# Kernel optimization log

Measured on AMD Instinct MI355X. Metric: run time of the kernel, lower is better.

Reference implementation:

```python
import jax, jax.numpy as jnp
import numpy as np

GW_EPS = 0.05
GW_SIGMA = 1.0
GW_OUTER_ITERS = 5
GW_SINK_ITERS = 20
N_HEADS = 8
EPS = 1e-8


def normalize_affinity(P):
    # symmetrize, scale to [0,1]
    P = 0.5 * (P + jnp.swapaxes(P, -1, -2))
    mx = jnp.max(P, axis=(-2, -1), keepdims=True)
    return P / jnp.maximum(mx, EPS)


def entropic_gw(C1, C2, a, b, eps, outer_iters, sink_iters):
    # C1: [B,H,S,S] node-space cost, C2: [B,H,K,K] slot-space cost
    # a: [B,H,S], b: [B,H,K] marginals. Square-loss entropic GW (Peyre et al.)
    T = a[..., :, None] * b[..., None, :]                      # [B,H,S,K]
    cC1 = jnp.einsum('bhij,bhj->bhi', C1 * C1, a)              # [B,H,S]
    cC2 = jnp.einsum('bhk,bhkl->bhl', b, C2 * C2)              # [B,H,K]
    const = cC1[..., :, None] + cC2[..., None, :]              # [B,H,S,K]
    tens = const
    for _ in range(outer_iters):
        tens = const - 2.0 * jnp.einsum('bhis,bhsk,bhlk->bhil', C1, T, C2)
        Kmat = jnp.exp(-tens / eps)
        u = jnp.ones_like(a)
        v = jnp.ones_like(b)
        def sink_step(carry, _):
            u, v = carry
            u = a / jnp.maximum(jnp.einsum('bhik,bhk->bhi', Kmat, v), 1e-30)
            v = b / jnp.maximum(jnp.einsum('bhik,bhi->bhk', Kmat, u), 1e-30)
            return (u, v), None
        (u, v), _ = jax.lax.scan(sink_step, (u, v), None, length=sink_iters)
        T = u[..., :, None] * Kmat * v[..., None, :]
    gw_val = jnp.sum(tens * T, axis=(-2, -1))                  # [B,H]
    return T, gw_val


def _forward(desc_embeddings, name_value_embeddings, shared_attn, prior_Q, DG, b, v_w, v_b):
    B, new_seq, D = name_value_embeddings.shape
    S = new_seq - 1
    H = N_HEADS
    hd = D // H

    # structural adjacency: CLS->Var on, Var->CLS off, Var-Var without self-loop
    var_adj = 1.0 - jnp.eye(S, dtype=name_value_embeddings.dtype)
    adj = jnp.zeros((new_seq, new_seq), dtype=name_value_embeddings.dtype)
    adj = adj.at[1:, 1:].set(var_adj)
    adj = adj.at[0, 1:].set(1.0)

    # Var-Var affinity from shared attention (detached in original)
    P_var = jax.lax.stop_gradient(shared_attn[:, :, 1:, 1:])   # [B,H,S,S]
    P_norm = normalize_affinity(P_var)
    DP = 1.0 - P_norm                                          # affinity -> distance

    deg_P = 0.5 * (P_norm.sum(-1) + P_norm.sum(-2))            # [B,H,S]
    a = deg_P / jnp.maximum(deg_P.sum(-1, keepdims=True), EPS)

    _, gw_val = entropic_gw(DP, DG, a, b, GW_EPS, GW_OUTER_ITERS, GW_SINK_ITERS)
    alpha = jnp.exp(-gw_val / GW_SIGMA)                        # [B,H] in (0,1]

    # sharpen prior Q by alpha (power sharpening + row renorm)
    Q_hat = jnp.power(jnp.maximum(prior_Q, EPS), 1.0 + alpha[..., None, None])
    Q_hat = Q_hat / jnp.maximum(Q_hat.sum(-1, keepdims=True), EPS)

    # embed Q_hat into CLS-augmented attention, mask, row-normalize
    slot = jnp.zeros((B, H, new_seq, new_seq), dtype=Q_hat.dtype)
    slot = slot.at[:, :, 1:, 1:].set(Q_hat)
    slot = slot.at[:, :, 0, 1:].set(1.0)
    slot = slot * adj[None, None]
    attn = slot / jnp.maximum(slot.sum(-1, keepdims=True), EPS)  # [B,H,S1,S1]

    v = name_value_embeddings @ v_w.T + v_b                    # [B,S1,D]
    v = v.reshape(B, new_seq, H, hd).transpose(0, 2, 1, 3)     # [B,H,S1,hd]
    context = jnp.einsum('bhij,bhjd->bhid', attn, v)
    basis_outputs = context.transpose(0, 2, 1, 3)              # [B,S1,H,hd]
    return basis_outputs, attn


def setup_inputs() -> dict:
    key = jax.random.key(0)
    ks = jax.random.split(key, 8)
    B, S1, D, H, K = 32, 385, 256, 8, 16
    S = S1 - 1
    desc = jax.random.normal(ks[0], (B, S, D), jnp.float32)
    nv = jax.random.normal(ks[1], (B, S1, D), jnp.float32)
    shared_attn = jax.nn.softmax(jax.random.normal(ks[2], (B, H, S1, S1), jnp.float32), axis=-1)
    prior_Q = jax.nn.softmax(jax.random.normal(ks[3], (B, H, S, S), jnp.float32), axis=-1)
    DG = jax.random.uniform(ks[4], (B, H, K, K), jnp.float32)
    DG = 0.5 * (DG + jnp.swapaxes(DG, -1, -2))
    b = jax.random.uniform(ks[5], (B, H, K), jnp.float32) + 0.1
    b = b / b.sum(-1, keepdims=True)
    v_w = jax.random.normal(ks[6], (D, D), jnp.float32) * (1.0 / np.sqrt(D))
    v_b = jnp.zeros((D,), jnp.float32)
    return {"desc_embeddings": desc, "name_value_embeddings": nv, "shared_attn": shared_attn,
            "prior_Q": prior_Q, "DG": DG, "b": b, "v_w": v_w, "v_b": v_b}


def reference(desc_embeddings, name_value_embeddings, shared_attn, prior_Q, DG, b, v_w, v_b):
    return _forward(desc_embeddings, name_value_embeddings, shared_attn, prior_Q, DG, b, v_w, v_b)
```

## Files before the change

### kernel.cpp

```cpp
#include <hip/hip_runtime.h>
#include <math.h>

constexpr int kS  = 384;
constexpr int kS1 = 385;
constexpr int kH  = 8;
constexpr int kB  = 32;
constexpr int kD  = 256;
constexpr float kEPS = 1e-8f;
constexpr float kNEG_INV_EPS_LOG2E = 28.853900817779268f;

__device__ __forceinline__ float waveReduceSum(float v) {
    #pragma unroll
    for (int m = 1; m < 64; m <<= 1) v += __shfl_xor(v, m);
    return v;
}
__device__ __forceinline__ float waveReduceMax(float v) {
    #pragma unroll
    for (int m = 1; m < 64; m <<= 1) v = fmaxf(v, __shfl_xor(v, m));
    return v;
}

__device__ __forceinline__ size_t symBase(int head) {
    return (size_t)head * (kS1 * kS1) + (size_t)((4 - (head & 3)) & 3);
}

__global__ __launch_bounds__(256) void k1a_sym(
    const float* __restrict__ shared_attn,
    float* __restrict__ sym_ws)
{
    const int head = blockIdx.y;
    const int ti   = blockIdx.x;
    const int tid  = threadIdx.x;
    const int c    = tid & 63;
    const int w    = tid >> 6;

    __shared__ float tB[64 * 65];
    __shared__ float wredA[4];

    const float* P = shared_attn + (size_t)head * (kS1 * kS1);
    float* SYM = sym_ws + symBase(head);
    float* rs  = SYM + kS * kS;
    float* mxs = rs + kS;

    float rs_part[16];
    #pragma unroll
    for (int k = 0; k < 16; ++k) rs_part[k] = 0.f;
    float mymax = 0.f;

    for (int tj = 0; tj < 6; ++tj) {
        __syncthreads();
        for (int e = tid; e < 4096; e += 256) {
            int r = e >> 6, cc = e & 63;
            tB[r * 65 + cc] = P[(size_t)(1 + tj * 64 + r) * kS1 + (1 + ti * 64 + cc)];
        }
        __syncthreads();
        #pragma unroll
        for (int k = 0; k < 16; ++k) {
            int r = w + 4 * k;
            float av = P[(size_t)(1 + ti * 64 + r) * kS1 + (1 + tj * 64 + c)];
            float v  = 0.5f * (av + tB[c * 65 + r]);
            mymax = fmaxf(mymax, v);
            rs_part[k] += v;
            SYM[(size_t)(ti * 64 + r) * kS + tj * 64 + c] = v;
        }
    }
    #pragma unroll
    for (int k = 0; k < 16; ++k) {
        float s = waveReduceSum(rs_part[k]);
        if (c == 0) rs[ti * 64 + w + 4 * k] = s;
    }
    float wm = waveReduceMax(mymax);
    if (c == 0) wredA[w] = wm;
    __syncthreads();
    if (tid == 0)
        mxs[ti] = fmaxf(fmaxf(wredA[0], wredA[1]), fmaxf(wredA[2], wredA[3]));
}

__global__ __launch_bounds__(384) void k1b_gw(
    const float* __restrict__ DG,
    const float* __restrict__ bmarg,
    float* __restrict__ sym_ws,
    float* __restrict__ alpha_out)
{
    const int head = blockIdx.x;
    const int tid  = threadIdx.x;
    const int lane = tid & 63, wid = tid >> 6;

    __shared__ __align__(16) float Ms[kS * 16];
    __shared__ float ravu[kS];
    __shared__ float part[6 * 16];
    __shared__ float C2l[256];
    __shared__ float bl16[16], cb16[16], cC216[16], vls[16];
    __shared__ float wred[6];

    float* SYM = sym_ws + symBase(head);
    const float* rs  = SYM + kS * kS;
    const float* mxp = rs + kS;

    if (tid < 256) C2l[tid] = DG[head * 256 + tid];
    if (tid >= 256 && tid < 272) bl16[tid - 256] = bmarg[head * 16 + (tid - 256)];

    const float tloc = rs[tid];
    float tw = waveReduceSum(tloc);
    if (lane == 0) wred[wid] = tw;
    __syncthreads();
    const float total = wred[0] + wred[1] + wred[2] + wred[3] + wred[4] + wred[5];
    const float mx = fmaxf(fmaxf(fmaxf(mxp[0], mxp[1]), fmaxf(mxp[2], mxp[3])),
                           fmaxf(mxp[4], mxp[5]));
    const float den_mx = fmaxf(mx, kEPS);
    const float inv_mx = 1.0f / den_mx;
    const float Sdeg   = total * inv_mx;
    const float den_a  = fmaxf(Sdeg, kEPS);
    const float a_reg  = (tloc * inv_mx) / den_a;
    ravu[tid] = a_reg;

    if (tid < 16) {
        float cb = 0.f, cc2 = 0.f;
        #pragma unroll
        for (int k = 0; k < 16; ++k) {
            cb += bl16[k] * C2l[tid * 16 + k];
            float c2 = C2l[k * 16 + tid];
            cc2 = fmaf(bl16[k] * c2, c2, cc2);
        }
        cb16[tid] = cb; cC216[tid] = cc2;
    }
    __syncthreads();

    const float4* __restrict__ symrow = (const float4*)(SYM + (size_t)tid * kS);
    float t1 = 0.f, t2 = 0.f;
    #pragma unroll 4
    for (int s4 = 0; s4 < 96; ++s4) {
        float4 v4 = symrow[s4];
        const float* av = &ravu[s4 * 4];
        float dp;
        dp = fmaf(-inv_mx, v4.x, 1.0f); t1 = fmaf(dp, av[0], t1); t2 = fmaf(dp * dp, av[0], t2);
        dp = fmaf(-inv_mx, v4.y, 1.0f); t1 = fmaf(dp, av[1], t1); t2 = fmaf(dp * dp, av[1], t2);
        dp = fmaf(-inv_mx, v4.z, 1.0f); t1 = fmaf(dp, av[2], t1); t2 = fmaf(dp * dp, av[2], t2);
        dp = fmaf(-inv_mx, v4.w, 1.0f); t1 = fmaf(dp, av[3], t1); t2 = fmaf(dp * dp, av[3], t2);
    }
    const float cc1 = t2;

    float kreg[16], vreg[16];
    float u_i = 0.f;
    #pragma unroll
    for (int l = 0; l < 16; ++l)
        kreg[l] = exp2f((cc1 + cC216[l] - 2.0f * cb16[l] * t1) * (-kNEG_INV_EPS_LOG2E));

    auto sinkhorn = [&]() {
        #pragma unroll
        for (int l = 0; l < 16; ++l) vreg[l] = 1.0f;
        for (int it = 0; it < 20; ++it) {
            float su = 0.f;
            #pragma unroll
            for (int l = 0; l < 16; ++l) su = fmaf(kreg[l], vreg[l], su);
            u_i = a_reg / fmaxf(su, 1e-30f);
            #pragma unroll
            for (int l = 0; l < 16; ++l) {
                float t = waveReduceSum(kreg[l] * u_i);
                if (lane == 0) part[wid * 16 + l] = t;
            }
            __syncthreads();
            if (tid < 16) {
                float dn = part[tid] + part[16 + tid] + part[32 + tid] +
                           part[48 + tid] + part[64 + tid] + part[80 + tid];
                vls[tid] = bl16[tid] / fmaxf(dn, 1e-30f);
            }
            __syncthreads();
            #pragma unroll
            for (int l = 0; l < 16; ++l) vreg[l] = vls[l];
        }
    };

    sinkhorn();

    float tens16[16];
    #pragma unroll
    for (int l = 0; l < 16; ++l) tens16[l] = 0.f;

    for (int outer = 1; outer < 5; ++outer) {
        {
            float wk[16];
            #pragma unroll
            for (int k = 0; k < 16; ++k) wk[k] = kreg[k] * vreg[k];
            float m[16];
            #pragma unroll
            for (int l = 0; l < 16; ++l) {
                float acc = 0.f;
                #pragma unroll
                for (int k = 0; k < 16; ++k) acc = fmaf(wk[k], C2l[l * 16 + k], acc);
                m[l] = acc * u_i;
            }
            float4* Ms4w = (float4*)Ms;
            Ms4w[tid * 4 + 0] = make_float4(m[0],  m[1],  m[2],  m[3]);
            Ms4w[tid * 4 + 1] = make_float4(m[4],  m[5],  m[6],  m[7]);
            Ms4w[tid * 4 + 2] = make_float4(m[8],  m[9],  m[10], m[11]);
            Ms4w[tid * 4 + 3] = make_float4(m[12], m[13], m[14], m[15]);
        }
        __syncthreads();
        float rd[16];
        #pragma unroll
        for (int l = 0; l < 16; ++l) rd[l] = 0.f;
        {
            const float4* Ms4 = (const float4*)Ms;
            #pragma unroll 2
            for (int s4 = 0; s4 < 96; ++s4) {
                float4 v4 = symrow[s4];
                #pragma unroll
                for (int j = 0; j < 4; ++j) {
                    float sym = (j == 0) ? v4.x : (j == 1) ? v4.y : (j == 2) ? v4.z : v4.w;
                    float dp = fmaf(-inv_mx, sym, 1.0f);
                    const int s = s4 * 4 + j;
                    float4 m0 = Ms4[s * 4 + 0];
                    float4 m1 = Ms4[s * 4 + 1];
                    float4 m2 = Ms4[s * 4 + 2];
                    float4 m3 = Ms4[s * 4 + 3];
                    rd[0]  = fmaf(dp, m0.x, rd[0]);  rd[1]  = fmaf(dp, m0.y, rd[1]);
                    rd[2]  = fmaf(dp, m0.z, rd[2]);  rd[3]  = fmaf(dp, m0.w, rd[3]);
                    rd[4]  = fmaf(dp, m1.x, rd[4]);  rd[5]  = fmaf(dp, m1.y, rd[5]);
                    rd[6]  = fmaf(dp, m1.z, rd[6]);  rd[7]  = fmaf(dp, m1.w, rd[7]);
                    rd[8]  = fmaf(dp, m2.x, rd[8]);  rd[9]  = fmaf(dp, m2.y, rd[9]);
                    rd[10] = fmaf(dp, m2.z, rd[10]); rd[11] = fmaf(dp, m2.w, rd[11]);
                    rd[12] = fmaf(dp, m3.x, rd[12]); rd[13] = fmaf(dp, m3.y, rd[13]);
                    rd[14] = fmaf(dp, m3.z, rd[14]); rd[15] = fmaf(dp, m3.w, rd[15]);
                }
            }
        }
        #pragma unroll
        for (int l = 0; l < 16; ++l) {
            float tens = cc1 + cC216[l] - 2.0f * rd[l];
            if (outer == 4) tens16[l] = tens;
            kreg[l] = exp2f(tens * (-kNEG_INV_EPS_LOG2E));
        }
        sinkhorn();
    }

    float g = 0.f;
    #pragma unroll
    for (int l = 0; l < 16; ++l) g = fmaf(tens16[l] * kreg[l], vreg[l], g);
    g *= u_i;
    float gww = waveReduceSum(g);
    if (lane == 0) wred[wid] = gww;
    __syncthreads();
    if (tid == 0) {
        float gw = wred[0] + wred[1] + wred[2] + wred[3] + wred[4] + wred[5];
        alpha_out[head] = expf(-gw);
    }
}

__global__ __launch_bounds__(256) void k2_attn(
    const float* __restrict__ priorQ,
    const float* __restrict__ alpha_in,
    float* __restrict__ attn_out)
{
    const int tid  = threadIdx.x;
    const int lane = tid & 63, wid = tid >> 6;
    const int head = blockIdx.x / 97;
    const int i    = (blockIdx.x % 97) * 4 + wid;
    if (i >= kS1) return;
    float* row = attn_out + (size_t)head * (kS1 * kS1) + (size_t)i * kS1;
    if (i == 0) {
        const float val = 1.0f / 384.0f;
        for (int j = lane; j < kS1; j += 64) row[j] = (j == 0) ? 0.f : val;
        return;
    }
    const float e = 1.0f + alpha_in[head];
    const float* q = priorQ + (size_t)head * (kS * kS) + (size_t)(i - 1) * kS;
    float p[6];
    float loc = 0.f, locd = 0.f;
    #pragma unroll
    for (int k = 0; k < 6; ++k) {
        int j = lane + k * 64;
        float qv = fmaxf(q[j], kEPS);
        float pv = exp2f(e * log2f(qv));
        p[k] = pv;
        loc += pv;
        if (j == i - 1) locd = pv;
    }
    float sum = loc, pd = locd;
    #pragma unroll
    for (int m = 1; m < 64; m <<= 1) { sum += __shfl_xor(sum, m); pd += __shfl_xor(pd, m); }
    const float qsum  = fmaxf(sum, kEPS);
    const float srow  = (sum - pd) / qsum;
    const float scale = 1.0f / (qsum * fmaxf(srow, kEPS));
    if (lane == 0) row[0] = 0.f;
    #pragma unroll
    for (int k = 0; k < 6; ++k) {
        int j = lane + k * 64;
        row[1 + j] = (j == i - 1) ? 0.f : p[k] * scale;
    }
}

__global__ __launch_bounds__(256) void k3_vproj(
    const float* __restrict__ nv,
    const float* __restrict__ vw,
    const float* __restrict__ vb,
    float* __restrict__ vfull)
{
    __shared__ float At[64][17];
    __shared__ float Bt[256][17];
    const int tid = threadIdx.x;
    const int r0  = blockIdx.x * 64;
    const int tx  = tid & 31;
    const int ty  = tid >> 5;
    const int M   = kB * kS1;
    float acc[8][8];
    #pragma unroll
    for (int ri = 0; ri < 8; ++ri)
        #pragma unroll
        for (int ci = 0; ci < 8; ++ci) acc[ri][ci] = 0.f;

    for (int k0 = 0; k0 < 256; k0 += 16) {
        __syncthreads();
        for (int e = tid; e < 1024; e += 256) {
            int r = e >> 4, kk = e & 15;
            int rowi = r0 + r;
            At[r][kk] = (rowi < M) ? nv[rowi * 256 + k0 + kk] : 0.f;
        }
        for (int e = tid; e < 4096; e += 256) {
            int c = e >> 4, kk = e & 15;
            Bt[c][kk] = vw[c * 256 + k0 + kk];
        }
        __syncthreads();
        #pragma unroll
        for (int kk = 0; kk < 16; ++kk) {
            float av[8], bv[8];
            #pragma unroll
            for (int ri = 0; ri < 8; ++ri) av[ri] = At[ty * 8 + ri][kk];
            #pragma unroll
            for (int ci = 0; ci < 8; ++ci) bv[ci] = Bt[tx + 32 * ci][kk];
            #pragma unroll
            for (int ri = 0; ri < 8; ++ri)
                #pragma unroll
                for (int ci = 0; ci < 8; ++ci)
                    acc[ri][ci] = fmaf(av[ri], bv[ci], acc[ri][ci]);
        }
    }
    for (int ri = 0; ri < 8; ++ri) {
        int rowi = r0 + ty * 8 + ri;
        if (rowi < M) {
            #pragma unroll
            for (int ci = 0; ci < 8; ++ci) {
                int c = tx + 32 * ci;
                vfull[rowi * 256 + c] = acc[ri][ci] + vb[c];
            }
        }
    }
}

__global__ __launch_bounds__(256) void k4_ctx(
    const float* __restrict__ attn,
    const float* __restrict__ vfull,
    float* __restrict__ basis)
{
    __shared__ __align__(16) float at[8 * 16 * 36];
    __shared__ __align__(16) float vt[32 * 256];
    const int tid = threadIdx.x;
    const int bb  = blockIdx.y;
    const int i0  = blockIdx.x * 16;
    const int h   = tid >> 5;
    float acc[16];
    #pragma unroll
    for (int i = 0; i < 16; ++i) acc[i] = 0.f;
    const float* attnB = attn + (size_t)bb * kH * kS1 * kS1;
    const float* vB    = vfull + (size_t)bb * kS1 * 256;

    for (int j0 = 0; j0 < kS1; j0 += 32) {
        __syncthreads();
        for (int e = tid; e < 4096; e += 256) {
            int jj = e & 31, ii = (e >> 5) & 15, hh = e >> 9;
            int gi = i0 + ii, gj = j0 + jj;
            at[(hh * 16 + ii) * 36 + jj] = (gi < kS1 && gj < kS1)
                ? attnB[(size_t)hh * kS1 * kS1 + (size_t)gi * kS1 + gj] : 0.f;
        }
        for (int e = tid; e < 2048; e += 256) {
            int c4 = e & 63, jr = e >> 6;
            int gj = j0 + jr;
            float4 vv = (gj < kS1) ? *(const float4*)&vB[(size_t)gj * 256 + c4 * 4]
                                   : make_float4(0.f, 0.f, 0.f, 0.f);
            *(float4*)&vt[jr * 256 + c4 * 4] = vv;
        }
        __syncthreads();
        #pragma unroll
        for (int j4 = 0; j4 < 8; ++j4) {
            float v0 = vt[(j4 * 4 + 0) * 256 + tid];
            float v1 = vt[(j4 * 4 + 1) * 256 + tid];
            float v2 = vt[(j4 * 4 + 2) * 256 + tid];
            float v3 = vt[(j4 * 4 + 3) * 256 + tid];
            #pragma unroll
            for (int i = 0; i < 16; ++i) {
                float4 av = *(const float4*)&at[(h * 16 + i) * 36 + j4 * 4];
                acc[i] = fmaf(av.x, v0, fmaf(av.y, v1, fmaf(av.z, v2, fmaf(av.w, v3, acc[i]))));
            }
        }
    }
    #pragma unroll
    for (int i = 0; i < 16; ++i) {
        int gi = i0 + i;
        if (gi < kS1) basis[((size_t)bb * kS1 + gi) * 256 + tid] = acc[i];
    }
}

extern "C" void kernel_launch(void* const* d_in, const int* in_sizes, int n_in,
                              void* d_out, int out_size, void* d_ws, size_t ws_size,
                              hipStream_t stream) {
    (void)in_sizes; (void)n_in; (void)out_size; (void)ws_size;
    const float* nv    = (const float*)d_in[1];
    const float* sattn = (const float*)d_in[2];
    const float* pq    = (const float*)d_in[3];
    const float* dg    = (const float*)d_in[4];
    const float* bm    = (const float*)d_in[5];
    const float* vw    = (const float*)d_in[6];
    const float* vb    = (const float*)d_in[7];

    float* out   = (float*)d_out;
    float* basis = out;
    float* attn  = out + (size_t)kB * kS1 * kD;
    float* alpha = (float*)d_ws;
    float* vfull = (float*)((char*)d_ws + 4096);

    k1a_sym<<<dim3(6, 256), 256, 0, stream>>>(sattn, attn);
    k1b_gw<<<256, 384, 0, stream>>>(dg, bm, attn, alpha);
    k2_attn<<<256 * 97, 256, 0, stream>>>(pq, alpha, attn);
    k3_vproj<<<193, 256, 0, stream>>>(nv, vw, vb, vfull);
    k4_ctx<<<dim3(25, 32), 256, 0, stream>>>(attn, vfull, basis);
}
```

Measured before the change: 1.322 ms.

## Split GW row reductions across two thread halves with interleaved SYM layout

The symmetric affinity workspace is now stored in a float4-interleaved column-major layout, so consecutive threads read consecutive float4s and the loads coalesce. The GW kernel block grows from 384 to 768 threads. Each half handles half of the reduction over s for the cost terms and the C1·M product, and the partial sums are combined through shared memory. Sinkhorn iterations still run only on the lower half. This targets the memory-bound row scans of the 256-block kernel, at the cost of more barriers, more shared memory and idle upper-half threads during Sinkhorn.

Result: no change. 1.303 ms (-1.4%).

```diff
diff --git a/kernel.cpp b/kernel.cpp
--- a/kernel.cpp
+++ b/kernel.cpp
@@ -38,9 +38,9 @@
     __shared__ float wredA[4];
 
     const float* P = shared_attn + (size_t)head * (kS1 * kS1);
-    float* SYM = sym_ws + symBase(head);
-    float* rs  = SYM + kS * kS;
-    float* mxs = rs + kS;
+    float* SYMp = sym_ws + symBase(head);
+    float* rs   = SYMp + kS * kS;
+    float* mxs  = rs + kS;
 
     float rs_part[16];
     #pragma unroll
@@ -54,6 +54,8 @@
             tB[r * 65 + cc] = P[(size_t)(1 + tj * 64 + r) * kS1 + (1 + ti * 64 + cc)];
         }
         __syncthreads();
+        const int col = tj * 64 + c;
+        const int s4  = col >> 2, cj = col & 3;
         #pragma unroll
         for (int k = 0; k < 16; ++k) {
             int r = w + 4 * k;
@@ -61,7 +63,7 @@
             float v  = 0.5f * (av + tB[c * 65 + r]);
             mymax = fmaxf(mymax, v);
             rs_part[k] += v;
-            SYM[(size_t)(ti * 64 + r) * kS + tj * 64 + c] = v;
+            SYMp[(size_t)(s4 * kS + ti * 64 + r) * 4 + cj] = v;
         }
     }
     #pragma unroll
@@ -76,7 +78,7 @@
         mxs[ti] = fmaxf(fmaxf(wredA[0], wredA[1]), fmaxf(wredA[2], wredA[3]));
 }
 
-__global__ __launch_bounds__(384) void k1b_gw(
+__global__ __launch_bounds__(768) void k1b_gw(
     const float* __restrict__ DG,
     const float* __restrict__ bmarg,
     float* __restrict__ sym_ws,
@@ -85,24 +87,31 @@
     const int head = blockIdx.x;
     const int tid  = threadIdx.x;
     const int lane = tid & 63, wid = tid >> 6;
+    const bool lower = (tid < kS);
+    const int  i     = lower ? tid : tid - kS;
+    const int  half  = lower ? 0 : 1;
 
     __shared__ __align__(16) float Ms[kS * 16];
+    __shared__ __align__(16) float pbuf[kS * 20];
     __shared__ float ravu[kS];
     __shared__ float part[6 * 16];
     __shared__ float C2l[256];
     __shared__ float bl16[16], cb16[16], cC216[16], vls[16];
     __shared__ float wred[6];
 
-    float* SYM = sym_ws + symBase(head);
-    const float* rs  = SYM + kS * kS;
+    float* SYMp = sym_ws + symBase(head);
+    const float* rs  = SYMp + kS * kS;
     const float* mxp = rs + kS;
 
     if (tid < 256) C2l[tid] = DG[head * 256 + tid];
     if (tid >= 256 && tid < 272) bl16[tid - 256] = bmarg[head * 16 + (tid - 256)];
 
-    const float tloc = rs[tid];
-    float tw = waveReduceSum(tloc);
-    if (lane == 0) wred[wid] = tw;
+    float a_reg = 0.f, tloc = 0.f;
+    if (lower) {
+        tloc = rs[i];
+        float tw = waveReduceSum(tloc);
+        if (lane == 0) wred[wid] = tw;
+    }
     __syncthreads();
     const float total = wred[0] + wred[1] + wred[2] + wred[3] + wred[4] + wred[5];
     const float mx = fmaxf(fmaxf(fmaxf(mxp[0], mxp[1]), fmaxf(mxp[2], mxp[3])),
@@ -111,9 +120,10 @@
     const float inv_mx = 1.0f / den_mx;
     const float Sdeg   = total * inv_mx;
     const float den_a  = fmaxf(Sdeg, kEPS);
-    const float a_reg  = (tloc * inv_mx) / den_a;
-    ravu[tid] = a_reg;
-
+    if (lower) {
+        a_reg = (tloc * inv_mx) / den_a;
+        ravu[i] = a_reg;
+    }
     if (tid < 16) {
         float cb = 0.f, cc2 = 0.f;
         #pragma unroll
@@ -126,11 +136,13 @@
     }
     __syncthreads();
 
-    const float4* __restrict__ symrow = (const float4*)(SYM + (size_t)tid * kS);
+    const float4* __restrict__ symp = (const float4*)SYMp;
+    const int s4beg = half * 48, s4end = s4beg + 48;
+
     float t1 = 0.f, t2 = 0.f;
-    #pragma unroll 4
-    for (int s4 = 0; s4 < 96; ++s4) {
-        float4 v4 = symrow[s4];
+    #pragma unroll 2
+    for (int s4 = s4beg; s4 < s4end; ++s4) {
+        float4 v4 = symp[s4 * kS + i];
         const float* av = &ravu[s4 * 4];
         float dp;
         dp = fmaf(-inv_mx, v4.x, 1.0f); t1 = fmaf(dp, av[0], t1); t2 = fmaf(dp * dp, av[0], t2);
@@ -138,26 +150,34 @@
         dp = fmaf(-inv_mx, v4.z, 1.0f); t1 = fmaf(dp, av[2], t1); t2 = fmaf(dp * dp, av[2], t2);
         dp = fmaf(-inv_mx, v4.w, 1.0f); t1 = fmaf(dp, av[3], t1); t2 = fmaf(dp * dp, av[3], t2);
     }
-    const float cc1 = t2;
+    if (!lower) { pbuf[i] = t1; pbuf[512 + i] = t2; }
+    __syncthreads();
 
     float kreg[16], vreg[16];
-    float u_i = 0.f;
-    #pragma unroll
-    for (int l = 0; l < 16; ++l)
-        kreg[l] = exp2f((cc1 + cC216[l] - 2.0f * cb16[l] * t1) * (-kNEG_INV_EPS_LOG2E));
+    float u_i = 0.f, cc1 = 0.f;
+    if (lower) {
+        t1 += pbuf[i];
+        t2 += pbuf[512 + i];
+        cc1 = t2;
+        #pragma unroll
+        for (int l = 0; l < 16; ++l)
+            kreg[l] = exp2f((cc1 + cC216[l] - 2.0f * cb16[l] * t1) * (-kNEG_INV_EPS_LOG2E));
+    }
 
     auto sinkhorn = [&]() {
         #pragma unroll
         for (int l = 0; l < 16; ++l) vreg[l] = 1.0f;
         for (int it = 0; it < 20; ++it) {
-            float su = 0.f;
-            #pragma unroll
-            for (int l = 0; l < 16; ++l) su = fmaf(kreg[l], vreg[l], su);
-            u_i = a_reg / fmaxf(su, 1e-30f);
-            #pragma unroll
-            for (int l = 0; l < 16; ++l) {
-                float t = waveReduceSum(kreg[l] * u_i);
-                if (lane == 0) part[wid * 16 + l] = t;
+            if (lower) {
+                float su = 0.f;
+                #pragma unroll
+                for (int l = 0; l < 16; ++l) su = fmaf(kreg[l], vreg[l], su);
+                u_i = a_reg / fmaxf(su, 1e-30f);
+                #pragma unroll
+                for (int l = 0; l < 16; ++l) {
+                    float t = waveReduceSum(kreg[l] * u_i);
+                    if (lane == 0) part[wid * 16 + l] = t;
+                }
             }
             __syncthreads();
             if (tid < 16) {
@@ -178,7 +198,7 @@
     for (int l = 0; l < 16; ++l) tens16[l] = 0.f;
 
     for (int outer = 1; outer < 5; ++outer) {
-        {
+        if (lower) {
             float wk[16];
             #pragma unroll
             for (int k = 0; k < 16; ++k) wk[k] = kreg[k] * vreg[k];
@@ -191,10 +211,10 @@
                 m[l] = acc * u_i;
             }
             float4* Ms4w = (float4*)Ms;
-            Ms4w[tid * 4 + 0] = make_float4(m[0],  m[1],  m[2],  m[3]);
-            Ms4w[tid * 4 + 1] = make_float4(m[4],  m[5],  m[6],  m[7]);
-            Ms4w[tid * 4 + 2] = make_float4(m[8],  m[9],  m[10], m[11]);
-            Ms4w[tid * 4 + 3] = make_float4(m[12], m[13], m[14], m[15]);
+            Ms4w[i * 4 + 0] = make_float4(m[0],  m[1],  m[2],  m[3]);
+            Ms4w[i * 4 + 1] = make_float4(m[4],  m[5],  m[6],  m[7]);
+            Ms4w[i * 4 + 2] = make_float4(m[8],  m[9],  m[10], m[11]);
+            Ms4w[i * 4 + 3] = make_float4(m[12], m[13], m[14], m[15]);
         }
         __syncthreads();
         float rd[16];
@@ -203,8 +223,8 @@
         {
             const float4* Ms4 = (const float4*)Ms;
             #pragma unroll 2
-            for (int s4 = 0; s4 < 96; ++s4) {
-                float4 v4 = symrow[s4];
+            for (int s4 = s4beg; s4 < s4end; ++s4) {
+                float4 v4 = symp[s4 * kS + i];
                 #pragma unroll
                 for (int j = 0; j < 4; ++j) {
                     float sym = (j == 0) ? v4.x : (j == 1) ? v4.y : (j == 2) ? v4.z : v4.w;
@@ -225,21 +245,39 @@
                 }
             }
         }
-        #pragma unroll
-        for (int l = 0; l < 16; ++l) {
-            float tens = cc1 + cC216[l] - 2.0f * rd[l];
-            if (outer == 4) tens16[l] = tens;
-            kreg[l] = exp2f(tens * (-kNEG_INV_EPS_LOG2E));
+        if (!lower) {
+            float4* pb = (float4*)&pbuf[i * 20];
+            pb[0] = make_float4(rd[0],  rd[1],  rd[2],  rd[3]);
+            pb[1] = make_float4(rd[4],  rd[5],  rd[6],  rd[7]);
+            pb[2] = make_float4(rd[8],  rd[9],  rd[10], rd[11]);
+            pb[3] = make_float4(rd[12], rd[13], rd[14], rd[15]);
+        }
+        __syncthreads();
+        if (lower) {
+            const float4* pb = (const float4*)&pbuf[i * 20];
+            float4 p0 = pb[0], p1 = pb[1], p2 = pb[2], p3 = pb[3];
+            rd[0] += p0.x; rd[1] += p0.y; rd[2]  += p0.z; rd[3]  += p0.w;
+            rd[4] += p1.x; rd[5] += p1.y; rd[6]  += p1.z; rd[7]  += p1.w;
+            rd[8] += p2.x; rd[9] += p2.y; rd[10] += p2.z; rd[11] += p2.w;
+            rd[12] += p3.x; rd[13] += p3.y; rd[14] += p3.z; rd[15] += p3.w;
+            #pragma unroll
+            for (int l = 0; l < 16; ++l) {
+                float tens = cc1 + cC216[l] - 2.0f * rd[l];
+                if (outer == 4) tens16[l] = tens;
+                kreg[l] = exp2f(tens * (-kNEG_INV_EPS_LOG2E));
+            }
         }
         sinkhorn();
     }
 
-    float g = 0.f;
-    #pragma unroll
-    for (int l = 0; l < 16; ++l) g = fmaf(tens16[l] * kreg[l], vreg[l], g);
-    g *= u_i;
-    float gww = waveReduceSum(g);
-    if (lane == 0) wred[wid] = gww;
+    if (lower) {
+        float g = 0.f;
+        #pragma unroll
+        for (int l = 0; l < 16; ++l) g = fmaf(tens16[l] * kreg[l], vreg[l], g);
+        g *= u_i;
+        float gww = waveReduceSum(g);
+        if (lane == 0) wred[wid] = gww;
+    }
     __syncthreads();
     if (tid == 0) {
         float gw = wred[0] + wred[1] + wred[2] + wred[3] + wred[4] + wred[5];
@@ -419,7 +457,7 @@
     float* vfull = (float*)((char*)d_ws + 4096);
 
     k1a_sym<<<dim3(6, 256), 256, 0, stream>>>(sattn, attn);
-    k1b_gw<<<256, 384, 0, stream>>>(dg, bm, attn, alpha);
+    k1b_gw<<<256, 768, 0, stream>>>(dg, bm, attn, alpha);
     k2_attn<<<256 * 97, 256, 0, stream>>>(pq, alpha, attn);
     k3_vproj<<<193, 256, 0, stream>>>(nv, vw, vb, vfull);
     k4_ctx<<<dim3(25, 32), 256, 0, stream>>>(attn, vfull, basis);
```
